# Kernel optimization log

Measured on AMD Instinct MI355X. Metric: run time of the kernel, lower is better.

The kernel has to match this reference:

```python
import jax, jax.numpy as jnp
import numpy as np

DIM = 8          # per-head dim
ATT_EPS = 1e-15
BN_EPS = 1e-6


def setup_inputs() -> dict:
    key = jax.random.key(0)
    ks = jax.random.split(key, 6)
    B, C, H, W = 8, 256, 64, 64
    td = 256                      # heads * dim = 32 * 8
    return {
        'x':      jax.random.normal(ks[0], (B, C, H, W), jnp.float32),
        'w_qkv':  jax.random.normal(ks[1], (3 * td, C), jnp.float32) * 0.05,
        'w_dw':   jax.random.normal(ks[2], (3 * td, 1, 5, 5), jnp.float32) * 0.05,
        'w_pw':   jax.random.normal(ks[3], (96, 8, 8), jnp.float32) * 0.05,   # (groups, out/g, in/g)
        'w_proj': jax.random.normal(ks[4], (C, 2 * td), jnp.float32) * 0.05,
        'bn_gamma': jnp.ones((C,), jnp.float32),
        'bn_beta':  jnp.zeros((C,), jnp.float32),
        'bn_mean':  jnp.zeros((C,), jnp.float32),
        'bn_var':   jnp.ones((C,), jnp.float32),
    }


def _relu_linear_att(ms, H, W):
    # ms: [B, C, H, W] with C = heads * 3*DIM
    B = ms.shape[0]
    d = DIM
    qkv = ms.reshape(B, -1, 3 * d, H * W).transpose(0, 1, 3, 2)   # [B, h, N, 3d]
    q = jax.nn.relu(qkv[..., :d])
    k = jax.nn.relu(qkv[..., d:2 * d])
    v = qkv[..., 2 * d:]
    v = jnp.pad(v, ((0, 0), (0, 0), (0, 0), (0, 1)), constant_values=1.0)  # ones column
    kv = jnp.einsum('bhnd,bhne->bhde', k, v)                       # [B, h, d, d+1]
    out = jnp.einsum('bhnd,bhde->bhne', q, kv)                     # [B, h, N, d+1]
    out = out[..., :-1] / (out[..., -1:] + ATT_EPS)
    return out.transpose(0, 1, 3, 2).reshape(B, -1, H, W)          # [B, h*d, H, W]


def reference(x, w_qkv, w_dw, w_pw, w_proj, bn_gamma, bn_beta, bn_mean, bn_var):
    B, C, H, W = x.shape
    # 1x1 qkv projection
    qkv = jnp.einsum('oc,bchw->bohw', w_qkv, x)                    # [B, 768, H, W]
    # multiscale aggregation: 5x5 depthwise then grouped 1x1 (groups = 3*heads = 96)
    dw = jax.lax.conv_general_dilated(
        qkv, w_dw, window_strides=(1, 1), padding=[(2, 2), (2, 2)],
        dimension_numbers=('NCHW', 'OIHW', 'NCHW'),
        feature_group_count=qkv.shape[1])
    G, O, I = w_pw.shape
    agg = jnp.einsum('goi,bgihw->bgohw', w_pw,
                     dw.reshape(B, G, I, H, W)).reshape(B, G * O, H, W)
    ms = jnp.concatenate([qkv, agg], axis=1)                       # [B, 1536, H, W]
    att = _relu_linear_att(ms, H, W)                               # [B, 512, H, W]
    # proj: 1x1 conv + BatchNorm (eval mode) + identity activation
    p = jnp.einsum('oc,bchw->bohw', w_proj, att)                   # [B, 256, H, W]
    inv = bn_gamma / jnp.sqrt(bn_var + BN_EPS)
    p = p * inv[None, :, None, None] + (bn_beta - bn_mean * inv)[None, :, None, None]
    return x + p
```

## Files before the change

kernel.cpp:

```cpp
#include <hip/hip_runtime.h>
#include <hip/hip_bf16.h>


#define HW 4096
#define ATT_EPS 1e-15f
#define BN_EPS 1e-6f

typedef __attribute__((ext_vector_type(8))) short short8;
typedef __attribute__((ext_vector_type(4))) short short4v;
typedef __attribute__((ext_vector_type(4))) float f32x4;
typedef __attribute__((ext_vector_type(2))) float f32x2;
typedef __attribute__((ext_vector_type(8))) unsigned short u16x8;
typedef __attribute__((ext_vector_type(4))) unsigned short u16x4;

static __device__ inline short f2bf(float f) {
    union { float f; unsigned u; } v; v.f = f;
    unsigned r = v.u + 0x7fff + ((v.u >> 16) & 1);
    return (short)(r >> 16);
}
static __device__ inline float bf2f(unsigned short u) {
    union { unsigned u; float f; } v; v.u = (unsigned)u << 16; return v.f;
}

static __device__ inline float dpp_shr1(float x) {
    int i = __builtin_bit_cast(int, x);
    int r = __builtin_amdgcn_update_dpp(0, i, 0x111, 0xF, 0xF, true);
    return __builtin_bit_cast(float, r);
}
static __device__ inline float dpp_shl1(float x) {
    int i = __builtin_bit_cast(int, x);
    int r = __builtin_amdgcn_update_dpp(0, i, 0x101, 0xF, 0xF, true);
    return __builtin_bit_cast(float, r);
}

__global__ __launch_bounds__(256) void prep_wb(const float* __restrict__ wproj,
                                               const float* __restrict__ wqkv,
                                               unsigned short* __restrict__ wbf,
                                               unsigned short* __restrict__ wqbf) {
    const int bid = blockIdx.x;
    const float* src;
    unsigned short* dst;
    int i;
    if (bid < 128) { src = wproj; dst = wbf;  i = (bid * 256 + threadIdx.x) * 4; }
    else           { src = wqkv;  dst = wqbf; i = ((bid - 128) * 256 + threadIdx.x) * 4; }
    float4 v = *(const float4*)&src[i];
    u16x4 r = {(unsigned short)f2bf(v.x), (unsigned short)f2bf(v.y),
               (unsigned short)f2bf(v.z), (unsigned short)f2bf(v.w)};
    *(u16x4*)&dst[i] = r;
}

__global__ __launch_bounds__(256) void prep_xt(const float* __restrict__ x,
                                               unsigned short* __restrict__ xt) {
    __shared__ unsigned short tl[64][72];
    const int b = blockIdx.z;
    const int c0 = blockIdx.y * 64, n0 = blockIdx.x * 64;
    const int t = threadIdx.x;
    const int nq = t & 15, cl = t >> 4;
#pragma unroll
    for (int p = 0; p < 4; p++) {
        const int c = cl + p * 16;
        float4 v = *(const float4*)&x[((size_t)b * 256 + c0 + c) * HW + n0 + nq * 4];
        tl[nq * 4 + 0][c] = (unsigned short)f2bf(v.x);
        tl[nq * 4 + 1][c] = (unsigned short)f2bf(v.y);
        tl[nq * 4 + 2][c] = (unsigned short)f2bf(v.z);
        tl[nq * 4 + 3][c] = (unsigned short)f2bf(v.w);
    }
    __syncthreads();
#pragma unroll
    for (int k = 0; k < 2; k++) {
        const int slot = t + 256 * k;
        const int nl = slot >> 3, oct = slot & 7;
        u16x8 v = *(const u16x8*)&tl[nl][oct * 8];
        *(u16x8*)&xt[((size_t)b * 4096 + n0 + nl) * 256 + c0 + oct * 8] = v;
    }
}

__global__ __launch_bounds__(256) void qkv_gemm(const unsigned short* __restrict__ xt,
                                                const unsigned short* __restrict__ wqbf,
                                                unsigned short* __restrict__ qkv) {
    __shared__ unsigned short A_l[128 * 40];
    __shared__ unsigned short B_l[128 * 40];
    const int t  = threadIdx.x;
    const int b  = blockIdx.z;
    const int ob = blockIdx.y * 128;
    const int nb = blockIdx.x * 128;
    const int lane = t & 63, wave = t >> 6;
    const int wo = (wave >> 1) * 64, wn = (wave & 1) * 64;
    const int am = lane & 15, ak = lane >> 4;

    const int r0 = t >> 2, c0 = t & 3;
    const unsigned short* asrc = wqbf + (size_t)(ob + r0) * 256 + c0 * 8;
    const unsigned short* bsrc = xt + ((size_t)b * 4096 + nb + r0) * 256 + c0 * 8;

    f32x4 acc[4][4];
#pragma unroll
    for (int s = 0; s < 4; s++)
#pragma unroll
        for (int u = 0; u < 4; u++) acc[s][u] = (f32x4){0.f, 0.f, 0.f, 0.f};

    u16x8 pa0, pa1, pb0, pb1;
#define QFETCH(KB)                                                             \
    {                                                                          \
        pa0 = *(const u16x8*)(asrc + (KB));                                    \
        pa1 = *(const u16x8*)(asrc + (size_t)64 * 256 + (KB));                 \
        pb0 = *(const u16x8*)(bsrc + (KB));                                    \
        pb1 = *(const u16x8*)(bsrc + (size_t)64 * 256 + (KB));                 \
    }

    QFETCH(0)
    for (int kb = 0; kb < 256; kb += 32) {
        __syncthreads();
        *(u16x8*)&A_l[r0 * 40 + c0 * 8]        = pa0;
        *(u16x8*)&A_l[(r0 + 64) * 40 + c0 * 8] = pa1;
        *(u16x8*)&B_l[r0 * 40 + c0 * 8]        = pb0;
        *(u16x8*)&B_l[(r0 + 64) * 40 + c0 * 8] = pb1;
        __syncthreads();

        if (kb + 32 < 256) QFETCH(kb + 32)

        short8 af[4], bf[4];
#pragma unroll
        for (int s = 0; s < 4; s++)
            af[s] = *(const short8*)&A_l[(wo + s * 16 + am) * 40 + ak * 8];
#pragma unroll
        for (int u = 0; u < 4; u++)
            bf[u] = *(const short8*)&B_l[(wn + u * 16 + am) * 40 + ak * 8];
#pragma unroll
        for (int s = 0; s < 4; s++)
#pragma unroll
            for (int u = 0; u < 4; u++)
                acc[s][u] = __builtin_amdgcn_mfma_f32_16x16x32_bf16(af[s], bf[u], acc[s][u], 0, 0, 0);
    }
#undef QFETCH

#pragma unroll
    for (int s = 0; s < 4; s++)
#pragma unroll
        for (int u = 0; u < 4; u++)
#pragma unroll
            for (int r = 0; r < 4; r++) {
                const int o = ob + wo + s * 16 + (lane >> 4) * 4 + r;
                const int nn = nb + wn + u * 16 + (lane & 15);
                qkv[((size_t)b * 768 + o) * HW + nn] = (unsigned short)f2bf(acc[s][u][r]);
            }
}

__global__ __launch_bounds__(256, 4) void dw_agg(const unsigned short* __restrict__ qkv,
                                                 const float* __restrict__ wdw,
                                                 const float* __restrict__ wpw,
                                                 unsigned short* __restrict__ agg) {
    __shared__ float tile[4 * 20 * 64];
    const int b = blockIdx.z, g = blockIdx.y;
    const int y0 = blockIdx.x * 16;
    const int t = threadIdx.x;
    const int tx = t & 15, ty = t >> 4;

    const float* wkg = wdw + g * 8 * 25;
    const float* pwg = wpw + g * 64;

    float out[8][4];
#pragma unroll
    for (int o = 0; o < 8; o++)
#pragma unroll
        for (int j = 0; j < 4; j++) out[o][j] = 0.f;

    u16x8 pf0, pf1, pf2;
#define DWFETCH(HALF)                                                          \
    {                                                                          \
        _Pragma("unroll")                                                      \
        for (int k = 0; k < 3; k++) {                                          \
            const int i = t + 256 * k;                                         \
            u16x8 v = {0, 0, 0, 0, 0, 0, 0, 0};                                \
            if (i < 640) {                                                     \
                const int c8 = i & 7, rr = (i >> 3) % 20, ch = i / 160;        \
                const int y = y0 - 2 + rr;                                     \
                if (y >= 0 && y < 64)                                          \
                    v = *(const u16x8*)&qkv[((size_t)(b * 768 + g * 8 + (HALF) * 4 + ch)) * HW + y * 64 + c8 * 8]; \
            }                                                                  \
            if (k == 0) pf0 = v; else if (k == 1) pf1 = v; else pf2 = v;       \
        }                                                                      \
    }

    DWFETCH(0)
#pragma unroll 1
    for (int half = 0; half < 2; half++) {
        if (half) __syncthreads();
#pragma unroll
        for (int k = 0; k < 3; k++) {
            const int i = t + 256 * k;
            if (i < 640) {
                u16x8 v = (k == 0) ? pf0 : (k == 1) ? pf1 : pf2;
                f32x4 lo = {bf2f(v[0]), bf2f(v[1]), bf2f(v[2]), bf2f(v[3])};
                f32x4 hi = {bf2f(v[4]), bf2f(v[5]), bf2f(v[6]), bf2f(v[7])};
                *(f32x4*)&tile[i * 8]     = lo;
                *(f32x4*)&tile[i * 8 + 4] = hi;
            }
        }
        __syncthreads();
        if (half == 0) DWFETCH(1)

#pragma unroll 2
        for (int ch4 = 0; ch4 < 4; ch4++) {
            const int ch = half * 4 + ch4;
            const float* wkc = wkg + ch * 25;
            float a0 = 0.f, a1 = 0.f, a2 = 0.f, a3 = 0.f;
#pragma unroll
            for (int dy = 0; dy < 5; dy++) {
                const int off = ch4 * 1280 + (ty + dy) * 64 + tx * 4;
                f32x4 C = *(const f32x4*)&tile[off];
                float win[8];
                win[0] = dpp_shr1(C[2]);
                win[1] = dpp_shr1(C[3]);
                win[2] = C[0]; win[3] = C[1];
                win[4] = C[2]; win[5] = C[3];
                win[6] = dpp_shl1(C[0]);
                win[7] = dpp_shl1(C[1]);
#pragma unroll
                for (int dx = 0; dx < 5; dx++) {
                    const float wv = wkc[dy * 5 + dx];
                    a0 += wv * win[dx + 0];
                    a1 += wv * win[dx + 1];
                    a2 += wv * win[dx + 2];
                    a3 += wv * win[dx + 3];
                }
            }
#pragma unroll
            for (int o = 0; o < 8; o++) {
                const float wv = pwg[o * 8 + ch];
                out[o][0] += wv * a0; out[o][1] += wv * a1;
                out[o][2] += wv * a2; out[o][3] += wv * a3;
            }
        }
    }
#undef DWFETCH

#pragma unroll
    for (int o = 0; o < 8; o++) {
        u16x4 rv = {(unsigned short)f2bf(out[o][0]), (unsigned short)f2bf(out[o][1]),
                    (unsigned short)f2bf(out[o][2]), (unsigned short)f2bf(out[o][3])};
        *(u16x4*)&agg[((size_t)(b * 768 + g * 8 + o)) * HW + (y0 + ty) * 64 + tx * 4] = rv;
    }
}

__global__ __launch_bounds__(256) void kv_pass(const unsigned short* __restrict__ qkv,
                                               const unsigned short* __restrict__ agg,
                                               float* __restrict__ kvpart) {
    const int t = threadIdx.x;
    const int w = t >> 6, lane = t & 63;
    const int hp = blockIdx.x * 4 + w;
    const int b = blockIdx.y, c = blockIdx.z;
    const int h0 = hp * 2, h1 = h0 + 1;
    const unsigned short* buf = (h0 < 32) ? qkv : agg;
    const int cb0 = (h0 & 31) * 24, cb1 = (h1 & 31) * 24;

    const int row = lane & 15, kgrp = lane >> 4;
    const int n0 = c * 256 + kgrp * 8;

    const int chA = (row < 8) ? (cb0 + 8 + row) : (cb1 + row);
    const unsigned short* ap = buf + ((size_t)b * 768 + chA) * HW + n0;

    const bool bload = (row < 8);
    const unsigned short* bp0 = buf + ((size_t)b * 768 + cb0 + 16 + (row & 7)) * HW + n0;
    const unsigned short* bp1 = buf + ((size_t)b * 768 + cb1 + 16 + (row & 7)) * HW + n0;
    const short cfill = (row == 8) ? (short)0x3F80 : (short)0;
    const short8 bconst = {cfill, cfill, cfill, cfill, cfill, cfill, cfill, cfill};

    f32x4 acc0 = {0.f, 0.f, 0.f, 0.f};
    f32x4 acc1 = {0.f, 0.f, 0.f, 0.f};

#pragma unroll
    for (int i = 0; i < 8; i++) {
        u16x8 av = *(const u16x8*)(ap + i * 32);
        short8 b0 = bload ? *(const short8*)(bp0 + i * 32) : bconst;
        short8 b1 = bload ? *(const short8*)(bp1 + i * 32) : bconst;
        short8 ar;
#pragma unroll
        for (int j = 0; j < 8; j++)
            ar[j] = (short)((av[j] & 0x8000) ? 0 : av[j]);
        acc0 = __builtin_amdgcn_mfma_f32_16x16x32_bf16(ar, b0, acc0, 0, 0, 0);
        acc1 = __builtin_amdgcn_mfma_f32_16x16x32_bf16(ar, b1, acc1, 0, 0, 0);
    }

    if (row <= 8) {
        float* kp;
        f32x4 a;
        int dbase;
        if (kgrp < 2) {
            kp = kvpart + (size_t)c * 36864 + (size_t)(b * 64 + h0) * 72;
            a = acc0; dbase = kgrp * 4;
        } else {
            kp = kvpart + (size_t)c * 36864 + (size_t)(b * 64 + h1) * 72;
            a = acc1; dbase = (kgrp - 2) * 4;
        }
#pragma unroll
        for (int r = 0; r < 4; r++)
            kp[(dbase + r) * 9 + row] = a[r];
    }
}

__global__ __launch_bounds__(256) void kv_red(const float* __restrict__ kvpart,
                                              float* __restrict__ kvout) {
    const int i = blockIdx.x * 256 + threadIdx.x;
    float s = 0.f;
#pragma unroll
    for (int c = 0; c < 16; c++) s += kvpart[(size_t)c * 36864 + i];
    kvout[i] = s;
}

__global__ __launch_bounds__(256) void att_pass(const unsigned short* __restrict__ qkv,
                                                const unsigned short* __restrict__ agg,
                                                const float* __restrict__ kvbuf,
                                                unsigned short* __restrict__ att_f) {
    const int h = blockIdx.y, b = blockIdx.z;
    const int t = threadIdx.x;
    const float* kvp = kvbuf + ((size_t)(b * 64 + h)) * 72;

    float kvr[72];
#pragma unroll
    for (int i = 0; i < 18; i++) {
        f32x4 v = *(const f32x4*)&kvp[i * 4];
        kvr[i * 4 + 0] = v[0]; kvr[i * 4 + 1] = v[1];
        kvr[i * 4 + 2] = v[2]; kvr[i * 4 + 3] = v[3];
    }

    const unsigned short* buf = (h < 32) ? qkv : agg;
    const int cbase = (h & 31) * 24;
    const int n0 = (blockIdx.x * 256 + t) * 8;
    const unsigned short* qp = buf + ((size_t)b * 768 + cbase) * HW + n0;

    float q[8][8];
#pragma unroll
    for (int d = 0; d < 8; d++) {
        u16x8 v = *(const u16x8*)&qp[(size_t)d * HW];
#pragma unroll
        for (int j = 0; j < 8; j++) q[d][j] = fmaxf(bf2f(v[j]), 0.f);
    }

    unsigned short* op = att_f + (((size_t)(b * 64 + h)) * HW + n0) * 8;
#pragma unroll
    for (int j = 0; j < 8; j++) {
        float num[9];
#pragma unroll
        for (int e = 0; e < 9; e++) num[e] = 0.f;
#pragma unroll
        for (int d = 0; d < 8; d++) {
            const float qv = q[d][j];
#pragma unroll
            for (int e = 0; e < 9; e++) num[e] += qv * kvr[d * 9 + e];
        }
        const float rden = 1.f / (num[8] + ATT_EPS);
        u16x8 r;
#pragma unroll
        for (int e = 0; e < 8; e++) r[e] = (unsigned short)f2bf(num[e] * rden);
        *(u16x8*)&op[j * 8] = r;
    }
}

__global__ __launch_bounds__(256) void proj_gemm(const unsigned short* __restrict__ wbf,
                                                 const unsigned short* __restrict__ att_f,
                                                 const float* __restrict__ gamma,
                                                 const float* __restrict__ beta,
                                                 const float* __restrict__ mean,
                                                 const float* __restrict__ var,
                                                 const float* __restrict__ x,
                                                 float* __restrict__ out) {
    const int t  = threadIdx.x;
    const int b  = blockIdx.z;
    const int ob = blockIdx.y * 128;
    const int nb = blockIdx.x * 128;
    const int lane = t & 63, wave = t >> 6;
    const int wo = (wave >> 1) * 64, wn = (wave & 1) * 64;

    const int am = lane & 15, ak = lane >> 4;
    const unsigned short* ap0 = wbf + (size_t)(ob + wo + am) * 512 + ak * 8;
    const unsigned short* bp0 = att_f +
        (((size_t)b * 64 + ak) * HW + nb + wn + am) * 8;

    f32x4 acc[4][4];
#pragma unroll
    for (int s = 0; s < 4; s++)
#pragma unroll
        for (int u = 0; u < 4; u++) acc[s][u] = (f32x4){0.f, 0.f, 0.f, 0.f};

    for (int kb = 0; kb < 512; kb += 32) {
        short8 af[4], bf[4];
#pragma unroll
        for (int s = 0; s < 4; s++)
            af[s] = *(const short8*)(ap0 + (size_t)s * 16 * 512 + kb);
#pragma unroll
        for (int u = 0; u < 4; u++)
            bf[u] = *(const short8*)(bp0 + ((size_t)(kb >> 3) * HW + u * 16) * 8);
#pragma unroll
        for (int s = 0; s < 4; s++)
#pragma unroll
            for (int u = 0; u < 4; u++)
                acc[s][u] = __builtin_amdgcn_mfma_f32_16x16x32_bf16(af[s], bf[u], acc[s][u], 0, 0, 0);
    }

#pragma unroll
    for (int s = 0; s < 4; s++) {
        const int o_base = ob + wo + s * 16 + (lane >> 4) * 4;
#pragma unroll
        for (int r = 0; r < 4; r++) {
            const int o = o_base + r;
            const float inv = gamma[o] * rsqrtf(var[o] + BN_EPS);
            const float sh  = beta[o] - mean[o] * inv;
#pragma unroll
            for (int u = 0; u < 4; u++) {
                const int n = nb + wn + u * 16 + (lane & 15);
                const size_t idx = ((size_t)b * 256 + o) * HW + n;
                out[idx] = x[idx] + acc[s][u][r] * inv + sh;
            }
        }
    }
}

extern "C" void kernel_launch(void* const* d_in, const int* in_sizes, int n_in,
                              void* d_out, int out_size, void* d_ws, size_t ws_size,
                              hipStream_t stream) {
    const float* x      = (const float*)d_in[0];
    const float* w_qkv  = (const float*)d_in[1];
    const float* w_dw   = (const float*)d_in[2];
    const float* w_pw   = (const float*)d_in[3];
    const float* w_proj = (const float*)d_in[4];
    const float* gamma  = (const float*)d_in[5];
    const float* beta   = (const float*)d_in[6];
    const float* mean   = (const float*)d_in[7];
    const float* var    = (const float*)d_in[8];
    float* out = (float*)d_out;

    unsigned short* qkv  = (unsigned short*)d_ws;
    unsigned short* agg  = qkv + (size_t)25165824;
    unsigned short* attf = agg + (size_t)25165824;
    unsigned short* wbf  = attf + (size_t)16777216;
    float* kvb = (float*)(wbf + (size_t)131072);
    float* kvpart = (float*)attf;
    unsigned short* wqbf = attf + (size_t)4194304;
    unsigned short* xt   = agg;

    prep_wb <<<dim3(320),       256, 0, stream>>>(w_proj, w_qkv, wbf, wqbf);
    prep_xt <<<dim3(64, 4, 8),  256, 0, stream>>>(x, xt);
    qkv_gemm<<<dim3(32, 6, 8),  256, 0, stream>>>(xt, wqbf, qkv);
    dw_agg  <<<dim3(4, 96, 8),  256, 0, stream>>>(qkv, w_dw, w_pw, agg);
    kv_pass <<<dim3(8, 8, 16),  256, 0, stream>>>(qkv, agg, kvpart);
    kv_red  <<<dim3(144),       256, 0, stream>>>(kvpart, kvb);
    att_pass<<<dim3(2, 64, 8),  256, 0, stream>>>(qkv, agg, kvb, attf);
    proj_gemm<<<dim3(32, 2, 8), 256, 0, stream>>>(wbf, attf,
                                                  gamma, beta, mean, var, x, out);
}
```

Measured before the change: 220.0 us.

## Stage proj GEMM tiles through LDS with register prefetch and smaller output tile

The projection GEMM now loads A and B k-slices cooperatively into padded shared memory and prefetches the next slice into registers while the current one is consumed. Before this, each wave read its MFMA fragments straight from global memory. The output tile per block shrinks from 128x128 to 64x128, so twice as many blocks launch and each thread holds fewer accumulators. The aim is coalesced, shared global loads and better occupancy, paid for with two barriers per k-step and more redundant B traffic across blocks.

```diff
diff --git a/kernel.cpp b/kernel.cpp
--- a/kernel.cpp
+++ b/kernel.cpp
@@ -364,50 +364,70 @@
                                                  const float* __restrict__ var,
                                                  const float* __restrict__ x,
                                                  float* __restrict__ out) {
+    __shared__ unsigned short A_l[64 * 40];
+    __shared__ unsigned short B_l[128 * 40];
     const int t  = threadIdx.x;
     const int b  = blockIdx.z;
-    const int ob = blockIdx.y * 128;
+    const int ob = blockIdx.y * 64;
     const int nb = blockIdx.x * 128;
     const int lane = t & 63, wave = t >> 6;
-    const int wo = (wave >> 1) * 64, wn = (wave & 1) * 64;
-
+    const int wn = wave * 32;
     const int am = lane & 15, ak = lane >> 4;
-    const unsigned short* ap0 = wbf + (size_t)(ob + wo + am) * 512 + ak * 8;
-    const unsigned short* bp0 = att_f +
-        (((size_t)b * 64 + ak) * HW + nb + wn + am) * 8;
-
-    f32x4 acc[4][4];
+
+    const int srow = t >> 2, sc8 = t & 3;
+    const unsigned short* asrc = wbf + (size_t)(ob + srow) * 512 + sc8 * 8;
+    const unsigned short* bbase = att_f + (size_t)b * 64 * HW * 8;
+
+    f32x4 acc[4][2];
 #pragma unroll
     for (int s = 0; s < 4; s++)
 #pragma unroll
-        for (int u = 0; u < 4; u++) acc[s][u] = (f32x4){0.f, 0.f, 0.f, 0.f};
-
+        for (int u = 0; u < 2; u++) acc[s][u] = (f32x4){0.f, 0.f, 0.f, 0.f};
+
+    u16x8 pa, pb0, pb1;
+#define PFETCH(KB)                                                             \
+    {                                                                          \
+        pa  = *(const u16x8*)(asrc + (KB));                                    \
+        pb0 = *(const u16x8*)(bbase + (((size_t)((KB) >> 3) + sc8) * HW + nb + srow) * 8); \
+        pb1 = *(const u16x8*)(bbase + (((size_t)((KB) >> 3) + sc8) * HW + nb + srow + 64) * 8); \
+    }
+
+    PFETCH(0)
     for (int kb = 0; kb < 512; kb += 32) {
-        short8 af[4], bf[4];
+        __syncthreads();
+        *(u16x8*)&A_l[srow * 40 + sc8 * 8]        = pa;
+        *(u16x8*)&B_l[srow * 40 + sc8 * 8]        = pb0;
+        *(u16x8*)&B_l[(srow + 64) * 40 + sc8 * 8] = pb1;
+        __syncthreads();
+
+        if (kb + 32 < 512) PFETCH(kb + 32)
+
+        short8 af[4], bf[2];
 #pragma unroll
         for (int s = 0; s < 4; s++)
-            af[s] = *(const short8*)(ap0 + (size_t)s * 16 * 512 + kb);
-#pragma unroll
-        for (int u = 0; u < 4; u++)
-            bf[u] = *(const short8*)(bp0 + ((size_t)(kb >> 3) * HW + u * 16) * 8);
+            af[s] = *(const short8*)&A_l[(s * 16 + am) * 40 + ak * 8];
+#pragma unroll
+        for (int u = 0; u < 2; u++)
+            bf[u] = *(const short8*)&B_l[(wn + u * 16 + am) * 40 + ak * 8];
 #pragma unroll
         for (int s = 0; s < 4; s++)
 #pragma unroll
-            for (int u = 0; u < 4; u++)
+            for (int u = 0; u < 2; u++)
                 acc[s][u] = __builtin_amdgcn_mfma_f32_16x16x32_bf16(af[s], bf[u], acc[s][u], 0, 0, 0);
     }
+#undef PFETCH
 
 #pragma unroll
     for (int s = 0; s < 4; s++) {
-        const int o_base = ob + wo + s * 16 + (lane >> 4) * 4;
+        const int o_base = ob + s * 16 + (lane >> 4) * 4;
 #pragma unroll
         for (int r = 0; r < 4; r++) {
             const int o = o_base + r;
             const float inv = gamma[o] * rsqrtf(var[o] + BN_EPS);
             const float sh  = beta[o] - mean[o] * inv;
 #pragma unroll
-            for (int u = 0; u < 4; u++) {
-                const int n = nb + wn + u * 16 + (lane & 15);
+            for (int u = 0; u < 2; u++) {
+                const int n = nb + wn + u * 16 + am;
                 const size_t idx = ((size_t)b * 256 + o) * HW + n;
                 out[idx] = x[idx] + acc[s][u][r] * inv + sh;
             }
@@ -445,6 +465,6 @@
     kv_pass <<<dim3(8, 8, 16),  256, 0, stream>>>(qkv, agg, kvpart);
     kv_red  <<<dim3(144),       256, 0, stream>>>(kvpart, kvb);
     att_pass<<<dim3(2, 64, 8),  256, 0, stream>>>(qkv, agg, kvb, attf);
-    proj_gemm<<<dim3(32, 2, 8), 256, 0, stream>>>(wbf, attf,
+    proj_gemm<<<dim3(32, 4, 8), 256, 0, stream>>>(wbf, attf,
                                                   gamma, beta, mean, var, x, out);
 }
```

Result: no change. 218.3 us (-0.7%).
